# Optimization experiments

Measured on AMD Instinct MI355X. Metric: run time of the kernel, lower is better.

The kernel has to match this reference:

```python
import jax, jax.numpy as jnp
import numpy as np

IN_F = 2048
OUT_F = 4096
LOW_DIM = 2048
LL_W = OUT_F * IN_F      # 8388608 = 2**23, power of two
LL_B = OUT_F             # 4096 = 2**12


def fwht(v):
    """Fast Walsh-Hadamard transform over a 1-D power-of-two vector (unnormalized),
    matching fast_walsh_hadamard_torched (chunk+cat butterfly)."""
    n = v.shape[0]
    k = int(round(np.log2(n)))
    v = v.reshape((2,) * k)
    for i in range(k):  # loop over log2(n) butterfly stages, not data dims
        a, b = jnp.split(v, 2, axis=i)
        v = jnp.concatenate([a + b, a - b], axis=i)
    return v.reshape(n)


def fastfood(z, dim, BB, GG, Pi):
    """pad -> sign-mul -> WHT -> permute -> Gaussian-mul -> WHT -> slice+scale."""
    LL = BB.shape[0]
    zp = jnp.zeros((LL,), z.dtype).at[: z.shape[0]].set(z)
    m = fwht(BB * zp)
    m = m[Pi] * GG
    m = fwht(m)
    divisor = jnp.sqrt(LL * jnp.sum(GG * GG))
    return m[:dim] / (divisor * np.sqrt(float(dim) / LL))


def setup_inputs() -> dict:
    key = jax.random.key(0)
    ks = jax.random.split(key, 9)
    x = jax.random.normal(ks[0], (4096, IN_F), dtype=jnp.float32)
    low_dim_params = jax.random.normal(ks[1], (LOW_DIM,), dtype=jnp.float32)
    W0 = jax.random.normal(ks[2], (OUT_F, IN_F), dtype=jnp.float32) * 0.02
    b0 = jax.random.normal(ks[3], (OUT_F,), dtype=jnp.float32) * 0.02
    # BB: random +/-1 signs (torch: uniform_(0,2).long()*2-1)
    BB_w = jnp.where(jax.random.uniform(ks[4], (LL_W,)) < 0.5, -1.0, 1.0).astype(jnp.float32)
    GG_w = jax.random.normal(ks[5], (LL_W,), dtype=jnp.float32)
    BB_b = jnp.where(jax.random.uniform(ks[6], (LL_B,)) < 0.5, -1.0, 1.0).astype(jnp.float32)
    GG_b = jax.random.normal(ks[7], (LL_B,), dtype=jnp.float32)
    kp1, kp2 = jax.random.split(ks[8])
    Pi_w = jax.random.permutation(kp1, LL_W).astype(jnp.int64)
    Pi_b = jax.random.permutation(kp2, LL_B).astype(jnp.int64)
    return {"x": x, "low_dim_params": low_dim_params, "W0": W0, "b0": b0,
            "BB_w": BB_w, "GG_w": GG_w, "BB_b": BB_b, "GG_b": GG_b,
            "Pi_w": Pi_w, "Pi_b": Pi_b}


def reference(x, low_dim_params, W0, b0, BB_w, GG_w, BB_b, GG_b, Pi_w, Pi_b):
    # FastfoodWrapper.set_params: param = initial_value + fastfood(low_dim_params)
    dW = fastfood(low_dim_params, OUT_F * IN_F, BB_w, GG_w, Pi_w).reshape(OUT_F, IN_F)
    db = fastfood(low_dim_params, OUT_F, BB_b, GG_b, Pi_b)
    W = W0 + dW
    b = b0 + db
    # base model forward: Linear
    return x @ W.T + b
```

## Files before the change

kernel.cpp:

```cpp
#include <hip/hip_runtime.h>
#include <hip/hip_bf16.h>
#include <math.h>

typedef __bf16  bf16x8 __attribute__((ext_vector_type(8)));
typedef float   f32x4  __attribute__((ext_vector_type(4)));

static __device__ __forceinline__ void load_lds16(const void* g, void* l) {
  __builtin_amdgcn_global_load_lds(
      (const __attribute__((address_space(1))) void*)(g),
      (__attribute__((address_space(3))) void*)(l), 16, 0, 0);
}

#define BAR() asm volatile("s_barrier" ::: "memory")
#define SB0() __builtin_amdgcn_sched_barrier(0)
#define LGKM(N) do { asm volatile("s_waitcnt lgkmcnt(" #N ")" ::: "memory"); SB0(); } while (0)
#define VMC(N) asm volatile("s_waitcnt vmcnt(" #N ")" ::: "memory")

static __device__ __forceinline__ float bf2f(unsigned short u) {
  unsigned int x = ((unsigned int)u) << 16;
  return __builtin_bit_cast(float, x);
}
static __device__ __forceinline__ unsigned short f2bf(float f) {
  __hip_bfloat16 h = __float2bfloat16(f);
  return *reinterpret_cast<unsigned short*>(&h);
}
static __device__ __forceinline__ unsigned pack2bf(float lo, float hi) {
  return (unsigned)f2bf(lo) | ((unsigned)f2bf(hi) << 16);
}

__global__ __launch_bounds__(256, 4) void k_mid1(
    const float* __restrict__ x, __hip_bfloat16* __restrict__ xb,
    const float* __restrict__ z, const float* __restrict__ BBw,
    const float* __restrict__ b0, const float* __restrict__ BBb,
    const float* __restrict__ GGb, const int* __restrict__ Pib,
    const int* __restrict__ Piw, const float* __restrict__ GGw,
    float* __restrict__ b_buf, float* __restrict__ Sw,
    __hip_bfloat16* __restrict__ m_buf) {
  __shared__ float S[4096];
  __shared__ float red[16];
  const int tid = threadIdx.x;
  const int bid = blockIdx.x;

  if (bid == 1024) {
    for (int i = tid; i < 4096; i += 256)
      S[i] = (i < 2048) ? BBb[i] * z[i] : 0.0f;
    float s = 0.0f;
    for (int i = tid; i < 4096; i += 256) { float g = GGb[i]; s += g * g; }
    for (int off = 32; off > 0; off >>= 1) s += __shfl_down(s, off);
    if ((tid & 63) == 0) red[tid >> 6] = s;
    __syncthreads();
    for (int len = 1; len < 4096; len <<= 1) {
      #pragma unroll
      for (int q = 0; q < 8; ++q) {
        int j = q * 256 + tid;
        int a = ((j & ~(len - 1)) << 1) | (j & (len - 1));
        float xx = S[a], y = S[a + len];
        S[a] = xx + y; S[a + len] = xx - y;
      }
      __syncthreads();
    }
    float v[16];
    #pragma unroll
    for (int q = 0; q < 16; ++q) v[q] = S[Pib[q * 256 + tid]] * GGb[q * 256 + tid];
    __syncthreads();
    #pragma unroll
    for (int q = 0; q < 16; ++q) S[q * 256 + tid] = v[q];
    __syncthreads();
    for (int len = 1; len < 4096; len <<= 1) {
      #pragma unroll
      for (int q = 0; q < 8; ++q) {
        int j = q * 256 + tid;
        int a = ((j & ~(len - 1)) << 1) | (j & (len - 1));
        float xx = S[a], y = S[a + len];
        S[a] = xx + y; S[a + len] = xx - y;
      }
      __syncthreads();
    }
    float Sb = red[0] + red[1] + red[2] + red[3];
    const float scale = 1.0f / sqrtf(Sb * 4096.0f);
    for (int i = tid; i < 4096; i += 256) b_buf[i] = b0[i] + S[i] * scale;
    return;
  }

  const int gtid = bid * 256 + tid;
  const int q6 = tid & 63, w = tid >> 6;
  #pragma unroll
  for (int i = 0; i < 8; ++i) {
    int q = gtid + i * 262144;
    float4 xv = reinterpret_cast<const float4*>(x)[q];
    ushort4 pk = make_ushort4(f2bf(xv.x), f2bf(xv.y), f2bf(xv.z), f2bf(xv.w));
    reinterpret_cast<ushort4*>(xb)[q] = pk;
  }

  {
    float v[8];
    float4 b0v = *reinterpret_cast<const float4*>(&BBw[tid * 8]);
    float4 b1v = *reinterpret_cast<const float4*>(&BBw[tid * 8 + 4]);
    float4 z0v = *reinterpret_cast<const float4*>(&z[tid * 8]);
    float4 z1v = *reinterpret_cast<const float4*>(&z[tid * 8 + 4]);
    v[0] = b0v.x * z0v.x; v[1] = b0v.y * z0v.y;
    v[2] = b0v.z * z0v.z; v[3] = b0v.w * z0v.w;
    v[4] = b1v.x * z1v.x; v[5] = b1v.y * z1v.y;
    v[6] = b1v.z * z1v.z; v[7] = b1v.w * z1v.w;
    #pragma unroll
    for (int st = 0; st < 3; ++st) {
      const int len = 1 << st;
      float t2[8];
      #pragma unroll
      for (int k = 0; k < 8; ++k) {
        int p = k ^ len;
        t2[k] = (k & len) ? v[p] - v[k] : v[k] + v[p];
      }
      #pragma unroll
      for (int k = 0; k < 8; ++k) v[k] = t2[k];
    }
    #pragma unroll
    for (int st = 0; st < 6; ++st) {
      const int xm = 1 << st;
      #pragma unroll
      for (int k = 0; k < 8; ++k) {
        float s2 = __shfl_xor(v[k], xm, 64);
        v[k] = (tid & xm) ? s2 - v[k] : v[k] + s2;
      }
    }
    #pragma unroll
    for (int k = 0; k < 8; ++k) S[2048 + k * 256 + tid] = v[k];
    __syncthreads();
    #pragma unroll
    for (int k = 0; k < 8; ++k) {
      float e0 = S[2048 + k * 256 + q6];
      float e1 = S[2048 + k * 256 + 64 + q6];
      float e2 = S[2048 + k * 256 + 128 + q6];
      float e3 = S[2048 + k * 256 + 192 + q6];
      float t1 = (w & 1) ? e0 - e1 : e0 + e1;
      float t2 = (w & 1) ? e2 - e3 : e2 + e3;
      v[k] = (w & 2) ? t1 - t2 : t1 + t2;
    }
    __syncthreads();
    f32x4 w0 = { v[0], v[1], v[2], v[3] };
    f32x4 w1 = { v[4], v[5], v[6], v[7] };
    *reinterpret_cast<f32x4*>(&S[tid * 8])     = w0;
    *reinterpret_cast<f32x4*>(&S[tid * 8 + 4]) = w1;
    __syncthreads();
  }

  float ssum = 0.0f;
  for (int rr = 0; rr < 4; ++rr) {
    const size_t p0 = ((size_t)bid * 4 + rr) * 2048;
    float v[8];
    #pragma unroll
    for (int h = 0; h < 2; ++h) {
      int4   pv = *reinterpret_cast<const int4*>(&Piw[p0 + tid * 8 + h * 4]);
      float4 gv = *reinterpret_cast<const float4*>(&GGw[p0 + tid * 8 + h * 4]);
      v[h * 4 + 0] = S[pv.x & 2047] * gv.x;
      v[h * 4 + 1] = S[pv.y & 2047] * gv.y;
      v[h * 4 + 2] = S[pv.z & 2047] * gv.z;
      v[h * 4 + 3] = S[pv.w & 2047] * gv.w;
      ssum += gv.x * gv.x + gv.y * gv.y + gv.z * gv.z + gv.w * gv.w;
    }
    #pragma unroll
    for (int st = 0; st < 3; ++st) {
      const int len = 1 << st;
      float t2[8];
      #pragma unroll
      for (int k = 0; k < 8; ++k) {
        int p = k ^ len;
        t2[k] = (k & len) ? v[p] - v[k] : v[k] + v[p];
      }
      #pragma unroll
      for (int k = 0; k < 8; ++k) v[k] = t2[k];
    }
    #pragma unroll
    for (int st = 0; st < 6; ++st) {
      const int xm = 1 << st;
      #pragma unroll
      for (int k = 0; k < 8; ++k) {
        float s2 = __shfl_xor(v[k], xm, 64);
        v[k] = (tid & xm) ? s2 - v[k] : v[k] + s2;
      }
    }
    #pragma unroll
    for (int k = 0; k < 8; ++k) S[2048 + k * 256 + tid] = v[k];
    __syncthreads();
    #pragma unroll
    for (int k = 0; k < 8; ++k) {
      float e0 = S[2048 + k * 256 + q6];
      float e1 = S[2048 + k * 256 + 64 + q6];
      float e2 = S[2048 + k * 256 + 128 + q6];
      float e3 = S[2048 + k * 256 + 192 + q6];
      float t1 = (w & 1) ? e0 - e1 : e0 + e1;
      float t2 = (w & 1) ? e2 - e3 : e2 + e3;
      v[k] = (w & 2) ? t1 - t2 : t1 + t2;
    }
    ushort4 o0 = make_ushort4(f2bf(v[0]), f2bf(v[1]), f2bf(v[2]), f2bf(v[3]));
    ushort4 o1 = make_ushort4(f2bf(v[4]), f2bf(v[5]), f2bf(v[6]), f2bf(v[7]));
    *reinterpret_cast<ushort4*>(&m_buf[p0 + tid * 8])     = o0;
    *reinterpret_cast<ushort4*>(&m_buf[p0 + tid * 8 + 4]) = o1;
    __syncthreads();
  }
  for (int off = 32; off > 0; off >>= 1) ssum += __shfl_down(ssum, off);
  if ((tid & 63) == 0) red[w] = ssum;
  __syncthreads();
  if (tid == 0) atomicAdd(Sw, red[0] + red[1] + red[2] + red[3]);
}

__global__ __launch_bounds__(256, 2) void k_mid2(__hip_bfloat16* __restrict__ m_buf) {
  const int gtid = blockIdx.x * 256 + threadIdx.x;
  const int f2 = gtid & 1023, oh = gtid >> 10;
  unsigned* mp = reinterpret_cast<unsigned*>(m_buf);
  const size_t base = (size_t)oh * 65536 + (size_t)f2;
  float v0[64], v1[64];
  #pragma unroll
  for (int s = 0; s < 64; ++s) {
    unsigned u = mp[base + (size_t)s * 1024];
    v0[s] = bf2f((unsigned short)(u & 0xffff));
    v1[s] = bf2f((unsigned short)(u >> 16));
  }
  #pragma unroll
  for (int len = 1; len < 64; len <<= 1) {
    #pragma unroll
    for (int j = 0; j < 32; ++j) {
      int a = ((j & ~(len - 1)) << 1) | (j & (len - 1));
      float xx = v0[a], y = v0[a + len];
      v0[a] = xx + y; v0[a + len] = xx - y;
      float xx1 = v1[a], y1 = v1[a + len];
      v1[a] = xx1 + y1; v1[a + len] = xx1 - y1;
    }
  }
  #pragma unroll
  for (int s = 0; s < 64; ++s)
    mp[base + (size_t)s * 1024] = pack2bf(v0[s], v1[s]);
}

__global__ __launch_bounds__(256, 2) void k_mid3(const __hip_bfloat16* __restrict__ m_buf,
                                                 const float* __restrict__ W0,
                                                 const float* __restrict__ Sw,
                                                 __hip_bfloat16* __restrict__ Wb) {
  const int gtid = blockIdx.x * 256 + threadIdx.x;
  const int f2 = gtid & 1023, ol = gtid >> 10;
  const unsigned* mp = reinterpret_cast<const unsigned*>(m_buf);
  const size_t baseu = (size_t)ol * 1024 + (size_t)f2;
  float v0[64], v1[64];
  #pragma unroll
  for (int s = 0; s < 64; ++s) {
    unsigned u = mp[baseu + (size_t)s * 65536];
    v0[s] = bf2f((unsigned short)(u & 0xffff));
    v1[s] = bf2f((unsigned short)(u >> 16));
  }
  #pragma unroll
  for (int len = 1; len < 64; len <<= 1) {
    #pragma unroll
    for (int j = 0; j < 32; ++j) {
      int a = ((j & ~(len - 1)) << 1) | (j & (len - 1));
      float xx = v0[a], y = v0[a + len];
      v0[a] = xx + y; v0[a + len] = xx - y;
      float xx1 = v1[a], y1 = v1[a + len];
      v1[a] = xx1 + y1; v1[a + len] = xx1 - y1;
    }
  }
  const float scale = 1.0f / sqrtf((*Sw) * 8388608.0f);
  unsigned* wbu = reinterpret_cast<unsigned*>(Wb);
  #pragma unroll
  for (int s = 0; s < 64; ++s) {
    size_t eidx = ((size_t)ol * 2048 + (size_t)f2 * 2) + (size_t)s * 131072;
    float2 wv = *reinterpret_cast<const float2*>(&W0[eidx]);
    wbu[(eidx >> 1)] = pack2bf(wv.x + v0[s] * scale, wv.y + v1[s] * scale);
  }
}

__global__ __launch_bounds__(512, 2) void k_gemm(const __hip_bfloat16* __restrict__ A,
                                                 const __hip_bfloat16* __restrict__ B,
                                                 const float* __restrict__ bias,
                                                 float* __restrict__ C) {
  constexpr int K = 2048, N = 4096, NT = K / 64;
  __shared__ __hip_bfloat16 As[2][256 * 64];
  __shared__ __hip_bfloat16 Bs[2][256 * 64];
  const int tid = threadIdx.x;
  const int wave = tid >> 6, lane = tid & 63;
  const int bid = blockIdx.x;
  const int swz = (bid & 7) * 32 + (bid >> 3);
  const int row0 = (swz & 15) * 256;
  const int col0 = (swz >> 4) * 256;
  const int wr = wave >> 2, wc = wave & 3;
  const int srow = tid >> 3;
  const int gslot = (tid & 7) ^ (srow & 7);
  const int ldst = tid * 8;
  const int lr = lane & 15, lk = lane >> 4;

  f32x4 acc[8][4] = {};
  bf16x8 a0[4][2], a1[4][2], b0[2][2], b1[2][2];

  #define STAGE_A(BUF, KT, CH0)                                                 \
    { _Pragma("unroll") for (int c = 0; c < 2; ++c)                             \
        load_lds16(A + (size_t)(row0 + (CH0 + c) * 64 + srow) * K + (KT) * 64 + gslot * 8, \
                   &As[BUF][(CH0 + c) * 4096 + ldst]); }
  #define STAGE_B(BUF, KT, CH0)                                                 \
    { _Pragma("unroll") for (int c = 0; c < 2; ++c)                             \
        load_lds16(B + (size_t)(col0 + (CH0 + c) * 64 + srow) * K + (KT) * 64 + gslot * 8, \
                   &Bs[BUF][(CH0 + c) * 4096 + ldst]); }

  #define READ_A(DST, BUF, HALF)                                                \
    { _Pragma("unroll") for (int i = 0; i < 4; ++i)                             \
        _Pragma("unroll") for (int ks = 0; ks < 2; ++ks) {                      \
          int row = wr * 128 + (HALF) * 64 + i * 16 + lr;                       \
          DST[i][ks] = *(const bf16x8*)&As[BUF][row * 64 + (((ks * 4 + lk) ^ (row & 7)) * 8)]; } }
  #define READ_B(DST, BUF, HALF)                                                \
    { _Pragma("unroll") for (int j = 0; j < 2; ++j)                             \
        _Pragma("unroll") for (int ks = 0; ks < 2; ++ks) {                      \
          int row = wc * 64 + (HALF) * 32 + j * 16 + lr;                        \
          DST[j][ks] = *(const bf16x8*)&Bs[BUF][row * 64 + (((ks * 4 + lk) ^ (row & 7)) * 8)]; } }

  #define MFMA16(AF, BF, IO, JO)                                                \
    { __builtin_amdgcn_s_setprio(1);                                            \
      _Pragma("unroll") for (int i = 0; i < 4; ++i)                             \
        _Pragma("unroll") for (int j = 0; j < 2; ++j)                           \
          _Pragma("unroll") for (int ks = 0; ks < 2; ++ks)                      \
            acc[(IO) + i][(JO) + j] =                                           \
              __builtin_amdgcn_mfma_f32_16x16x32_bf16(AF[i][ks], BF[j][ks],     \
                                                      acc[(IO) + i][(JO) + j], 0, 0, 0); \
      __builtin_amdgcn_s_setprio(0); }

  STAGE_A(0, 0, 0) STAGE_B(0, 0, 0) STAGE_A(0, 0, 2) STAGE_B(0, 0, 2)
  STAGE_A(1, 1, 0)
  VMC(2);
  BAR();

  for (int it = 0; it < 16; ++it) {
    const int u = 2 * it;
    const int v = u + 1;
    const int u2 = (u + 2 < NT) ? u + 2 : NT - 1;
    const int u3 = (u + 3 < NT) ? u + 3 : NT - 1;

    READ_A(a0, 0, 0) READ_B(b0, 0, 0)
    STAGE_A(1, v, 2)
    LGKM(8);
    BAR(); LGKM(0);
    MFMA16(a0, b0, 0, 0)
    VMC(4);
    BAR();
    READ_B(b1, 0, 1)
    STAGE_B(1, v, 0)
    BAR(); LGKM(0);
    MFMA16(a0, b1, 0, 2)
    BAR();
    READ_A(a1, 0, 1)
    STAGE_B(1, v, 2)
    BAR(); LGKM(0);
    MFMA16(a1, b1, 4, 2)
    BAR();
    STAGE_A(0, u2, 0)
    BAR();
    MFMA16(a1, b0, 4, 0)
    VMC(4);
    BAR();

    READ_A(a0, 1, 0) READ_B(b0, 1, 0)
    STAGE_B(0, u2, 0)
    LGKM(8);
    BAR(); LGKM(0);
    MFMA16(a0, b0, 0, 0)
    VMC(4);
    BAR();
    READ_B(b1, 1, 1)
    STAGE_A(0, u2, 2)
    BAR(); LGKM(0);
    MFMA16(a0, b1, 0, 2)
    BAR();
    READ_A(a1, 1, 1)
    STAGE_B(0, u2, 2)
    BAR(); LGKM(0);
    MFMA16(a1, b1, 4, 2)
    BAR();
    STAGE_A(1, u3, 0)
    BAR();
    MFMA16(a1, b0, 4, 0)
    VMC(6);
    BAR();
  }

  VMC(0);
  float bv[4];
  #pragma unroll
  for (int j = 0; j < 4; ++j) bv[j] = bias[col0 + wc * 64 + j * 16 + lr];
  float* eps = (float*)&As[0][0];
  #pragma unroll
  for (int r = 0; r < 4; ++r) {
    BAR();
    if (wr == (r >> 1)) {
      const int i0 = (r & 1) * 4;
      #pragma unroll
      for (int i = 0; i < 4; ++i)
        #pragma unroll
        for (int j = 0; j < 4; ++j)
          #pragma unroll
          for (int q = 0; q < 4; ++q) {
            int lrow = i * 16 + lk * 4 + q;
            int col = wc * 64 + j * 16 + lr;
            int sc = ((((col >> 2) ^ (lrow & 7)) << 2) | (col & 3));
            eps[lrow * 256 + sc] = acc[i0 + i][j][q] + bv[j];
          }
    }
    BAR();
    #pragma unroll
    for (int s = 0; s < 8; ++s) {
      int idx = s * 512 + tid;
      int lrow = idx >> 6;
      int g = idx & 63;
      f32x4 vv = *(const f32x4*)&eps[lrow * 256 + ((g ^ (lrow & 7)) << 2)];
      *(f32x4*)&C[(size_t)(row0 + r * 64 + lrow) * N + col0 + g * 4] = vv;
    }
  }
  #undef STAGE_A
  #undef STAGE_B
  #undef READ_A
  #undef READ_B
  #undef MFMA16
}

extern "C" void kernel_launch(void* const* d_in, const int* in_sizes, int n_in,
                              void* d_out, int out_size, void* d_ws, size_t ws_size,
                              hipStream_t stream) {
  (void)in_sizes; (void)n_in; (void)out_size; (void)ws_size;
  const float* x   = (const float*)d_in[0];
  const float* z   = (const float*)d_in[1];
  const float* W0  = (const float*)d_in[2];
  const float* b0  = (const float*)d_in[3];
  const float* BBw = (const float*)d_in[4];
  const float* GGw = (const float*)d_in[5];
  const float* BBb = (const float*)d_in[6];
  const float* GGb = (const float*)d_in[7];
  const int*   Piw = (const int*)d_in[8];
  const int*   Pib = (const int*)d_in[9];
  float* out = (float*)d_out;

  char* ws = (char*)d_ws;
  float*    b_buf = (float*)(ws + 8192);
  float*    Sw    = (float*)(ws + 24576);
  __hip_bfloat16* m_buf = (__hip_bfloat16*)(ws + 32768);
  __hip_bfloat16* Wb = (__hip_bfloat16*)(ws + 32768 + 16777216);
  __hip_bfloat16* xb = (__hip_bfloat16*)(ws + 32768 + 16777216 + 16777216);

  hipMemsetAsync(ws + 24576, 0, 4, stream);
  k_mid1<<<1025, 256, 0, stream>>>(x, xb, z, BBw, b0, BBb, GGb, Pib, Piw, GGw,
                                   b_buf, Sw, m_buf);
  k_mid2<<<256, 256, 0, stream>>>(m_buf);
  k_mid3<<<256, 256, 0, stream>>>(m_buf, W0, Sw, Wb);
  k_gemm<<<256, 512, 0, stream>>>(xb, Wb, b_buf, out);
}
```

Baseline: 135.0 us.

## Replace atomic sum with per-block partials, move x conversion to k_mid2, drop GEMM swizzle

Each k_mid1 block now writes its partial sum of squares to its own slot, and k_mid2 block 0 reduces the partials. This removes the memset launch and the 1024 contended atomics. The x fp32-to-bf16 conversion moves from k_mid1 into k_mid2, so k_mid1 only does the gather/transform work and k_mid2 gets more memory-bound work alongside its in-register butterflies. The GEMM block-index swizzle is also removed, which may change L2 reuse of A/B tiles.

```diff
diff --git a/kernel.cpp b/kernel.cpp
--- a/kernel.cpp
+++ b/kernel.cpp
@@ -29,12 +29,11 @@
 }
 
 __global__ __launch_bounds__(256, 4) void k_mid1(
-    const float* __restrict__ x, __hip_bfloat16* __restrict__ xb,
     const float* __restrict__ z, const float* __restrict__ BBw,
     const float* __restrict__ b0, const float* __restrict__ BBb,
     const float* __restrict__ GGb, const int* __restrict__ Pib,
     const int* __restrict__ Piw, const float* __restrict__ GGw,
-    float* __restrict__ b_buf, float* __restrict__ Sw,
+    float* __restrict__ b_buf, float* __restrict__ Sw_part,
     __hip_bfloat16* __restrict__ m_buf) {
   __shared__ float S[4096];
   __shared__ float red[16];
@@ -82,15 +81,7 @@
     return;
   }
 
-  const int gtid = bid * 256 + tid;
   const int q6 = tid & 63, w = tid >> 6;
-  #pragma unroll
-  for (int i = 0; i < 8; ++i) {
-    int q = gtid + i * 262144;
-    float4 xv = reinterpret_cast<const float4*>(x)[q];
-    ushort4 pk = make_ushort4(f2bf(xv.x), f2bf(xv.y), f2bf(xv.z), f2bf(xv.w));
-    reinterpret_cast<ushort4*>(xb)[q] = pk;
-  }
 
   {
     float v[8];
@@ -201,11 +192,32 @@
   for (int off = 32; off > 0; off >>= 1) ssum += __shfl_down(ssum, off);
   if ((tid & 63) == 0) red[w] = ssum;
   __syncthreads();
-  if (tid == 0) atomicAdd(Sw, red[0] + red[1] + red[2] + red[3]);
-}
-
-__global__ __launch_bounds__(256, 2) void k_mid2(__hip_bfloat16* __restrict__ m_buf) {
-  const int gtid = blockIdx.x * 256 + threadIdx.x;
+  if (tid == 0) Sw_part[bid] = red[0] + red[1] + red[2] + red[3];
+}
+
+__global__ __launch_bounds__(256, 2) void k_mid2(__hip_bfloat16* __restrict__ m_buf,
+                                                 const float* __restrict__ x,
+                                                 __hip_bfloat16* __restrict__ xb,
+                                                 const float* __restrict__ Sw_part,
+                                                 float* __restrict__ Sw) {
+  const int tid = threadIdx.x;
+  const int gtid = blockIdx.x * 256 + tid;
+  if (blockIdx.x == 0) {
+    float s = 0.0f;
+    for (int i = tid; i < 1024; i += 256) s += Sw_part[i];
+    for (int off = 32; off > 0; off >>= 1) s += __shfl_down(s, off);
+    __shared__ float r4[4];
+    if ((tid & 63) == 0) r4[tid >> 6] = s;
+    __syncthreads();
+    if (tid == 0) *Sw = r4[0] + r4[1] + r4[2] + r4[3];
+  }
+  #pragma unroll
+  for (int i = 0; i < 32; ++i) {
+    int q = gtid + i * 65536;
+    float4 xv = reinterpret_cast<const float4*>(x)[q];
+    ushort4 pk = make_ushort4(f2bf(xv.x), f2bf(xv.y), f2bf(xv.z), f2bf(xv.w));
+    reinterpret_cast<ushort4*>(xb)[q] = pk;
+  }
   const int f2 = gtid & 1023, oh = gtid >> 10;
   unsigned* mp = reinterpret_cast<unsigned*>(m_buf);
   const size_t base = (size_t)oh * 65536 + (size_t)f2;
@@ -278,9 +290,8 @@
   const int tid = threadIdx.x;
   const int wave = tid >> 6, lane = tid & 63;
   const int bid = blockIdx.x;
-  const int swz = (bid & 7) * 32 + (bid >> 3);
-  const int row0 = (swz & 15) * 256;
-  const int col0 = (swz >> 4) * 256;
+  const int row0 = (bid & 15) * 256;
+  const int col0 = (bid >> 4) * 256;
   const int wr = wave >> 2, wc = wave & 3;
   const int srow = tid >> 3;
   const int gslot = (tid & 7) ^ (srow & 7);
@@ -434,16 +445,16 @@
   float* out = (float*)d_out;
 
   char* ws = (char*)d_ws;
-  float*    b_buf = (float*)(ws + 8192);
-  float*    Sw    = (float*)(ws + 24576);
+  float*    b_buf   = (float*)(ws + 8192);
+  float*    Sw      = (float*)(ws + 24576);
+  float*    Sw_part = (float*)(ws + 28672);
   __hip_bfloat16* m_buf = (__hip_bfloat16*)(ws + 32768);
   __hip_bfloat16* Wb = (__hip_bfloat16*)(ws + 32768 + 16777216);
   __hip_bfloat16* xb = (__hip_bfloat16*)(ws + 32768 + 16777216 + 16777216);
 
-  hipMemsetAsync(ws + 24576, 0, 4, stream);
-  k_mid1<<<1025, 256, 0, stream>>>(x, xb, z, BBw, b0, BBb, GGb, Pib, Piw, GGw,
-                                   b_buf, Sw, m_buf);
-  k_mid2<<<256, 256, 0, stream>>>(m_buf);
+  k_mid1<<<1025, 256, 0, stream>>>(z, BBw, b0, BBb, GGb, Pib, Piw, GGw,
+                                   b_buf, Sw_part, m_buf);
+  k_mid2<<<256, 256, 0, stream>>>(m_buf, x, xb, Sw_part, Sw);
   k_mid3<<<256, 256, 0, stream>>>(m_buf, W0, Sw, Wb);
   k_gemm<<<256, 512, 0, stream>>>(xb, Wb, b_buf, out);
 }
```

New measurement: 127.8 us (median of 3 runs). -5.3%, faster.
